# Optimization experiments

Measured on AMD Instinct MI355X. Metric: run time of the kernel, lower is better.

## Reference

```python
import jax, jax.numpy as jnp
import numpy as np

H = 128        # hidden_dim
NP = 512       # program nodes
NV = 50000     # voxel nodes
E = 800000     # cross edges (16 per voxel)
TAU = 1.0
SLOPE = 0.01   # LeakyReLU default negative slope


def setup_inputs() -> dict:
    key = jax.random.key(0)
    ks = jax.random.split(key, 12)
    s = 1.0 / np.sqrt(H)
    x = jax.random.normal(ks[0], (NP, H), dtype=jnp.float32)
    v = jax.random.normal(ks[1], (NV, H), dtype=jnp.float32)
    row0 = jax.random.randint(ks[2], (E,), 0, NP, dtype=jnp.int32)
    row1 = (jnp.arange(E, dtype=jnp.int32) % NV)  # every voxel gets E/NV edges
    cross_edge_index = jnp.stack([row0, row1])    # [2, E]
    W_program = jax.random.normal(ks[3], (H, H), dtype=jnp.float32) * s
    b_program = jnp.zeros((H,), dtype=jnp.float32)
    W_voxel = jax.random.normal(ks[4], (H, H), dtype=jnp.float32) * s
    b_voxel = jnp.zeros((H,), dtype=jnp.float32)
    W_m1 = jax.random.normal(ks[5], (H, H), dtype=jnp.float32) * s
    b_m1 = jnp.zeros((H,), dtype=jnp.float32)
    W_m2 = jax.random.normal(ks[6], (H, 1), dtype=jnp.float32) * s
    b_m2 = jnp.zeros((1,), dtype=jnp.float32)
    theta = jax.random.normal(ks[7], (H, 1), dtype=jnp.float32) * s  # xavier-like
    u = jax.random.uniform(ks[8], (E,), dtype=jnp.float32)
    gumbel_u = jnp.clip(u, 1e-7, 1.0 - 1e-7)  # avoid log(0)
    return {"x": x, "v": v, "cross_edge_index": cross_edge_index,
            "W_program": W_program, "b_program": b_program,
            "W_voxel": W_voxel, "b_voxel": b_voxel,
            "W_m1": W_m1, "b_m1": b_m1, "W_m2": W_m2, "b_m2": b_m2,
            "theta": theta, "gumbel_u": gumbel_u}


def reference(x, v, cross_edge_index, W_program, b_program, W_voxel, b_voxel,
              W_m1, b_m1, W_m2, b_m2, theta, gumbel_u):
    src = cross_edge_index[0]
    dst = cross_edge_index[1]
    x_sel = x[src]                      # [E, H] gather
    v_sel = v[dst]                      # [E, H] gather
    # mask = sigmoid(MLP(v)) : Linear -> LeakyReLU -> Linear(H,1)
    a = v @ W_m1 + b_m1
    a = jnp.where(a >= 0, a, SLOPE * a)
    mask = jax.nn.sigmoid(a @ W_m2 + b_m2)                  # [NV, 1]
    # attention logits: theta^T * tanh(Wp x_sel + Wv v_sel), summed over H
    t = jnp.tanh(x_sel @ W_program + b_program + v_sel @ W_voxel + b_voxel)
    e = jnp.sum(t * theta[:, 0], axis=-1)                   # [E]
    # Gumbel softmax: global softmax over all edges (dim=0 in torch on 1-D e)
    g = -jnp.log(-jnp.log(gumbel_u))
    y = jax.nn.softmax((e + g) / TAU)                       # [E]
    # per-voxel hard argmax (scatter_max), straight-through estimator
    seg_max = jax.ops.segment_max(y, dst, num_segments=NV)  # [NV]
    is_max = y == seg_max[dst]
    cand = jnp.where(is_max, jnp.arange(E), E)
    argmax = jax.ops.segment_min(cand, dst, num_segments=NV)  # [NV], first max per voxel
    y_hard_1 = jnp.zeros(E + 1, y.dtype).at[argmax].set(1.0)[:E]  # overflow slot for empty segments
    y_hard = jax.lax.stop_gradient(y_hard_1 - y) + y
    # scatter-sum of soft-attended program features back to voxels
    summed = jax.ops.segment_sum(x_sel * y[:, None], dst, num_segments=NV)  # [NV, H]
    v_out = v + mask * summed
    return (v_out, mask, y[:, None], y_hard[:, None])
```

## Files before the change

kernel.cpp:

```cpp
#include <hip/hip_runtime.h>

#define H     128
#define NP    512
#define NVOX  50000
#define NEDGE 800000
#define EPV   16
#define SLOPE 0.01f
#define GR    32
#define NBLK  ((NVOX + GR - 1) / GR)
#define STRH  136
#define VSTR  132
#define C1    2.8853900817779268f
#define LOG2E 1.4426950408889634f
#define LN2   0.6931471805599453f
#define ABLK  3125

#define EXP2(x) __builtin_amdgcn_exp2f(x)
#define LOG2(x) __builtin_amdgcn_logf(x)
#define RCP(x)  __builtin_amdgcn_rcpf(x)

typedef _Float16 h16;
typedef __attribute__((ext_vector_type(4))) _Float16 h16x4;
typedef __attribute__((ext_vector_type(8))) _Float16 h16x8;
typedef __attribute__((ext_vector_type(4))) float    f32x4;

__global__ __launch_bounds__(256) void k_pre(const float* __restrict__ x,
                                             const float* __restrict__ Wp,
                                             const float* __restrict__ bp,
                                             const float* __restrict__ Wv,
                                             const float* __restrict__ Wm1,
                                             float* __restrict__ xpout,
                                             h16* __restrict__ WvThi,
                                             h16* __restrict__ WvTlo,
                                             h16* __restrict__ Wm1T) {
    __shared__ float part[H];
    int bid = blockIdx.x;
    int tid = threadIdx.x;
    if (bid < NP) {
        int row = bid;
        int col = tid & 127;
        int kh  = tid >> 7;
        int kbase = kh * 64;
        const float* xr = x + (size_t)row * H;
        float acc = 0.f;
#pragma unroll 8
        for (int k = 0; k < 64; ++k)
            acc = fmaf(xr[kbase + k], Wp[(size_t)(kbase + k) * H + col], acc);
        if (kh == 1) part[col] = acc;
        __syncthreads();
        if (kh == 0) xpout[(size_t)row * H + col] = (acc + part[col] + bp[col]) * C1;
    } else {
        int idx = (bid - NP) * 256 + tid;
        if (idx < 16384) {
            int k = idx >> 7, n = idx & 127;
            float w = Wv[idx];
            h16 hi = (h16)w;
            WvThi[n * H + k] = hi;
            WvTlo[n * H + k] = (h16)(w - (float)hi);
        } else {
            int j = idx - 16384;
            int k = j >> 7, n = j & 127;
            Wm1T[n * H + k] = (h16)Wm1[j];
        }
    }
}

__global__ __launch_bounds__(256, 2) void k_main(
    const float* __restrict__ v,   const float* __restrict__ x,
    const float* __restrict__ bv,  const float* __restrict__ bm1,
    const float* __restrict__ Wm2, const float* __restrict__ bm2,
    const h16* __restrict__ WvThi, const h16* __restrict__ WvTlo,
    const h16* __restrict__ Wm1T,
    const float* __restrict__ xp,  const int* __restrict__ cei,
    const float* __restrict__ theta, const float* __restrict__ gum,
    float* __restrict__ mask_out, float* __restrict__ pout,
    float* __restrict__ sump,     float* __restrict__ partial)
{
    __shared__ __align__(16) char ldsbuf[GR * STRH * 2 * 2];
    h16*   vh = (h16*)ldsbuf;
    h16*   vl = vh + GR * STRH;
    float* vt = (float*)ldsbuf;
    __shared__ float pmbuf[4][GR];
    __shared__ float psums[4];
    __shared__ float ptile[EPV][GR];
    __shared__ int   amtile[GR];

    int tid  = threadIdx.x;
    int base = blockIdx.x * GR;

#pragma unroll
    for (int i = 0; i < 4; ++i) {
        int f  = i * 256 + tid;
        int r  = f >> 5, c4 = f & 31;
        int gr = base + r;
        float4 val = (gr < NVOX) ? *(const float4*)&v[(size_t)gr * H + c4 * 4]
                                 : make_float4(0.f, 0.f, 0.f, 0.f);
        h16x4 hi, lo;
        hi.x = (h16)val.x; lo.x = (h16)(val.x - (float)hi.x);
        hi.y = (h16)val.y; lo.y = (h16)(val.y - (float)hi.y);
        hi.z = (h16)val.z; lo.z = (h16)(val.z - (float)hi.z);
        hi.w = (h16)val.w; lo.w = (h16)(val.w - (float)hi.w);
        *(h16x4*)&vh[r * STRH + c4 * 4] = hi;
        *(h16x4*)&vl[r * STRH + c4 * 4] = lo;
    }
    __syncthreads();

    int wave = tid >> 6, lane = tid & 63;
    int m16 = lane & 15, quad = lane >> 4;
    int cb = wave * 32;

    f32x4 aV[2][2], aM[2][2];
#pragma unroll
    for (int rt = 0; rt < 2; ++rt)
#pragma unroll
        for (int ct = 0; ct < 2; ++ct) { aV[rt][ct] = (f32x4)0.f; aM[rt][ct] = (f32x4)0.f; }

#pragma unroll
    for (int kc = 0; kc < 4; ++kc) {
        int kofs = kc * 32 + quad * 8;
        h16x8 ah[2], al[2];
#pragma unroll
        for (int rt = 0; rt < 2; ++rt) {
            int row = rt * 16 + m16;
            ah[rt] = *(const h16x8*)&vh[row * STRH + kofs];
            al[rt] = *(const h16x8*)&vl[row * STRH + kofs];
        }
#pragma unroll
        for (int ct = 0; ct < 2; ++ct) {
            int n = cb + ct * 16 + m16;
            h16x8 bh = *(const h16x8*)&WvThi[n * H + kofs];
            h16x8 bl = *(const h16x8*)&WvTlo[n * H + kofs];
            h16x8 bm = *(const h16x8*)&Wm1T[n * H + kofs];
#pragma unroll
            for (int rt = 0; rt < 2; ++rt) {
                aV[rt][ct] = __builtin_amdgcn_mfma_f32_16x16x32_f16(ah[rt], bh, aV[rt][ct], 0, 0, 0);
                aV[rt][ct] = __builtin_amdgcn_mfma_f32_16x16x32_f16(al[rt], bh, aV[rt][ct], 0, 0, 0);
                aV[rt][ct] = __builtin_amdgcn_mfma_f32_16x16x32_f16(ah[rt], bl, aV[rt][ct], 0, 0, 0);
                aM[rt][ct] = __builtin_amdgcn_mfma_f32_16x16x32_f16(ah[rt], bm, aM[rt][ct], 0, 0, 0);
            }
        }
    }
    __syncthreads();

    float pml[2][4];
#pragma unroll
    for (int rt = 0; rt < 2; ++rt)
#pragma unroll
        for (int reg = 0; reg < 4; ++reg) pml[rt][reg] = 0.f;
#pragma unroll
    for (int ct = 0; ct < 2; ++ct) {
        int col = cb + ct * 16 + m16;
        float bvc = bv[col], bmc = bm1[col], w2c = Wm2[col];
#pragma unroll
        for (int rt = 0; rt < 2; ++rt)
#pragma unroll
            for (int reg = 0; reg < 4; ++reg) {
                int row = rt * 16 + quad * 4 + reg;
                vt[row * VSTR + col] = (aV[rt][ct][reg] + bvc) * C1;
                float m = aM[rt][ct][reg] + bmc;
                m = (m >= 0.f) ? m : SLOPE * m;
                pml[rt][reg] = fmaf(m, w2c, pml[rt][reg]);
            }
    }
#pragma unroll
    for (int off = 8; off >= 1; off >>= 1)
#pragma unroll
        for (int rt = 0; rt < 2; ++rt)
#pragma unroll
            for (int reg = 0; reg < 4; ++reg)
                pml[rt][reg] += __shfl_xor(pml[rt][reg], off, 64);
    if (m16 == 0) {
#pragma unroll
        for (int rt = 0; rt < 2; ++rt)
#pragma unroll
            for (int reg = 0; reg < 4; ++reg)
                pmbuf[wave][rt * 16 + quad * 4 + reg] = pml[rt][reg];
    }
    __syncthreads();
    if (wave == 0 && lane < GR) {
        int gr = base + lane;
        if (gr < NVOX) {
            float s = pmbuf[0][lane] + pmbuf[1][lane] + pmbuf[2][lane]
                    + pmbuf[3][lane] + bm2[0];
            mask_out[gr] = RCP(1.f + EXP2(-s * LOG2E));
        }
    }

    int g = tid >> 3, lk = tid & 7;
    float th2[16], thsum = 0.f;
#pragma unroll
    for (int i = 0; i < 4; ++i) {
        float4 t4 = *(const float4*)&theta[(lk + 8 * i) * 4];
        th2[i * 4 + 0] = -2.f * t4.x; th2[i * 4 + 1] = -2.f * t4.y;
        th2[i * 4 + 2] = -2.f * t4.z; th2[i * 4 + 3] = -2.f * t4.w;
        thsum += t4.x + t4.y + t4.z + t4.w;
    }
    int vox = base + g;
    bool valid = vox < NVOX;
    const float* vr = &vt[g * VSTR];
    float4 b0 = *(const float4*)&vr[(lk +  0) * 4];
    float4 b1 = *(const float4*)&vr[(lk +  8) * 4];
    float4 b2 = *(const float4*)&vr[(lk + 16) * 4];
    float4 b3 = *(const float4*)&vr[(lk + 24) * 4];

    float4 s0 = make_float4(0.f,0.f,0.f,0.f), s1 = s0, s2 = s0, s3 = s0;
    float psum = 0.f, pmax = -1.f;
    int   pidx = 0;
#pragma unroll 2
    for (int t = 0; t < EPV; ++t) {
        int e   = vox + t * NVOX;
        int src = valid ? cei[e] : 0;
        const float4* xr = (const float4*)(xp + (size_t)src * H);
        const float4* xo = (const float4*)(x  + (size_t)src * H);
        float4 a0 = xr[lk], a1 = xr[lk + 8], a2 = xr[lk + 16], a3 = xr[lk + 24];
        float4 c0 = xo[lk], c1 = xo[lk + 8], c2 = xo[lk + 16], c3 = xo[lk + 24];
        float acc0 = thsum, acc1 = 0.f;
        acc0 = fmaf(th2[ 0], RCP(EXP2(a0.x + b0.x) + 1.f), acc0);
        acc1 = fmaf(th2[ 1], RCP(EXP2(a0.y + b0.y) + 1.f), acc1);
        acc0 = fmaf(th2[ 2], RCP(EXP2(a0.z + b0.z) + 1.f), acc0);
        acc1 = fmaf(th2[ 3], RCP(EXP2(a0.w + b0.w) + 1.f), acc1);
        acc0 = fmaf(th2[ 4], RCP(EXP2(a1.x + b1.x) + 1.f), acc0);
        acc1 = fmaf(th2[ 5], RCP(EXP2(a1.y + b1.y) + 1.f), acc1);
        acc0 = fmaf(th2[ 6], RCP(EXP2(a1.z + b1.z) + 1.f), acc0);
        acc1 = fmaf(th2[ 7], RCP(EXP2(a1.w + b1.w) + 1.f), acc1);
        acc0 = fmaf(th2[ 8], RCP(EXP2(a2.x + b2.x) + 1.f), acc0);
        acc1 = fmaf(th2[ 9], RCP(EXP2(a2.y + b2.y) + 1.f), acc1);
        acc0 = fmaf(th2[10], RCP(EXP2(a2.z + b2.z) + 1.f), acc0);
        acc1 = fmaf(th2[11], RCP(EXP2(a2.w + b2.w) + 1.f), acc1);
        acc0 = fmaf(th2[12], RCP(EXP2(a3.x + b3.x) + 1.f), acc0);
        acc1 = fmaf(th2[13], RCP(EXP2(a3.y + b3.y) + 1.f), acc1);
        acc0 = fmaf(th2[14], RCP(EXP2(a3.z + b3.z) + 1.f), acc0);
        acc1 = fmaf(th2[15], RCP(EXP2(a3.w + b3.w) + 1.f), acc1);
        float acc = acc0 + acc1;
        acc += __shfl_xor(acc, 4, 64);
        acc += __shfl_xor(acc, 2, 64);
        acc += __shfl_xor(acc, 1, 64);
        float u  = gum[valid ? e : 0];
        float gm = -LN2 * LOG2(-LN2 * LOG2(u));
        float p  = EXP2((acc + gm) * LOG2E);
        if (p > pmax) { pmax = p; pidx = t; }
        psum += (lk == 0 && valid) ? p : 0.f;
        if (lk == 0) ptile[t][g] = p;
        s0.x = fmaf(p, c0.x, s0.x); s0.y = fmaf(p, c0.y, s0.y);
        s0.z = fmaf(p, c0.z, s0.z); s0.w = fmaf(p, c0.w, s0.w);
        s1.x = fmaf(p, c1.x, s1.x); s1.y = fmaf(p, c1.y, s1.y);
        s1.z = fmaf(p, c1.z, s1.z); s1.w = fmaf(p, c1.w, s1.w);
        s2.x = fmaf(p, c2.x, s2.x); s2.y = fmaf(p, c2.y, s2.y);
        s2.z = fmaf(p, c2.z, s2.z); s2.w = fmaf(p, c2.w, s2.w);
        s3.x = fmaf(p, c3.x, s3.x); s3.y = fmaf(p, c3.y, s3.y);
        s3.z = fmaf(p, c3.z, s3.z); s3.w = fmaf(p, c3.w, s3.w);
    }
    if (lk == 0) amtile[g] = pidx;
    if (valid) {
        float* sr = sump + (size_t)vox * H;
        *(float4*)&sr[(lk +  0) * 4] = s0;
        *(float4*)&sr[(lk +  8) * 4] = s1;
        *(float4*)&sr[(lk + 16) * 4] = s2;
        *(float4*)&sr[(lk + 24) * 4] = s3;
    }
    __syncthreads();
#pragma unroll
    for (int it = 0; it < 2; ++it) {
        int t = (tid >> 5) + 8 * it, c = tid & 31;
        int vox2 = base + c;
        if (vox2 < NVOX) {
            float val = ptile[t][c];
            pout[vox2 + t * NVOX] = (t == amtile[c]) ? -val : val;
        }
    }
#pragma unroll
    for (int off = 32; off >= 1; off >>= 1) psum += __shfl_xor(psum, off, 64);
    if (lane == 0) psums[wave] = psum;
    __syncthreads();
    if (tid == 0)
        partial[blockIdx.x] = psums[0] + psums[1] + psums[2] + psums[3];
}

__global__ __launch_bounds__(256) void k_out(const float* __restrict__ v,
                                             const float* __restrict__ maskp,
                                             const float* __restrict__ partial,
                                             float* __restrict__ vout,
                                             float* __restrict__ ybuf,
                                             float* __restrict__ yhard) {
    __shared__ float red[4];
    int tid = threadIdx.x;
    float s = 0.f;
    for (int i = tid; i < NBLK; i += 256) s += partial[i];
#pragma unroll
    for (int off = 32; off >= 1; off >>= 1) s += __shfl_xor(s, off, 64);
    if ((tid & 63) == 0) red[tid >> 6] = s;
    __syncthreads();
    float invS = RCP(red[0] + red[1] + red[2] + red[3]);

    int bid = blockIdx.x;
    if (bid < ABLK) {
#pragma unroll
        for (int r = 0; r < 2; ++r) {
            int i = (bid + r * ABLK) * 256 + tid;
            float4 sp = ((const float4*)vout)[i];
            float4 vv = ((const float4*)v)[i];
            float  m  = maskp[i >> 5] * invS;
            float4 o;
            o.x = fmaf(m, sp.x, vv.x); o.y = fmaf(m, sp.y, vv.y);
            o.z = fmaf(m, sp.z, vv.z); o.w = fmaf(m, sp.w, vv.w);
            ((float4*)vout)[i] = o;
        }
    } else {
        int e = (bid - ABLK) * 256 + tid;
        float pv = ybuf[e];
        ybuf[e]  = fabsf(pv) * invS;
        yhard[e] = (pv < 0.f) ? 1.f : 0.f;
    }
}

extern "C" void kernel_launch(void* const* d_in, const int* in_sizes, int n_in,
                              void* d_out, int out_size, void* d_ws, size_t ws_size,
                              hipStream_t stream) {
    (void)in_sizes; (void)n_in; (void)out_size; (void)ws_size;
    const float* x   = (const float*)d_in[0];
    const float* v   = (const float*)d_in[1];
    const int*   cei = (const int*)d_in[2];
    const float* Wp  = (const float*)d_in[3];
    const float* bp  = (const float*)d_in[4];
    const float* Wv  = (const float*)d_in[5];
    const float* bv  = (const float*)d_in[6];
    const float* Wm1 = (const float*)d_in[7];
    const float* bm1 = (const float*)d_in[8];
    const float* Wm2 = (const float*)d_in[9];
    const float* bm2 = (const float*)d_in[10];
    const float* th  = (const float*)d_in[11];
    const float* gum = (const float*)d_in[12];

    float* out   = (float*)d_out;
    float* vout  = out;
    float* maskp = out + (size_t)NVOX * H;
    float* ybuf  = maskp + NVOX;
    float* yhard = ybuf + NEDGE;
    float* xp    = yhard;
    h16*   WvThi = (h16*)(yhard + 65536);
    h16*   WvTlo = WvThi + 16384;
    h16*   Wm1T  = WvThi + 32768;
    float* partial = (float*)d_ws;

    k_pre<<<NP + 128, 256, 0, stream>>>(x, Wp, bp, Wv, Wm1, xp, WvThi, WvTlo, Wm1T);
    k_main<<<NBLK, 256, 0, stream>>>(v, x, bv, bm1, Wm2, bm2, WvThi, WvTlo, Wm1T,
                                     xp, cei, th, gum, maskp, ybuf, vout, partial);
    k_out<<<2 * ABLK, 256, 0, stream>>>(v, maskp, partial, vout, ybuf, yhard);
}
```

Measured before the change: 192.5 us.

## Halve voxels per block, split edges across thread halves, stage indices in LDS

Each block now handles 16 voxels instead of 32. The 16 edges per voxel are split between two halves of the block, and the two partial scatter sums are combined through shared memory. Edge indices and gumbel values are prefetched into LDS, and the gumbel term is folded into a multiplicative weight computed with fewer transcendentals. The partial-sum reduction moves out of every k_out block into a single k_reduce kernel. The aim is more blocks and more parallelism per voxel, at the cost of an extra launch, extra syncs, and dependence on NVOX being divisible by 16.

Result: slower. 197.4 us (+2.5%).

```diff
diff --git a/kernel.cpp b/kernel.cpp
--- a/kernel.cpp
+++ b/kernel.cpp
@@ -6,13 +6,12 @@
 #define NEDGE 800000
 #define EPV   16
 #define SLOPE 0.01f
-#define GR    32
-#define NBLK  ((NVOX + GR - 1) / GR)
+#define GR    16
+#define NBLK  (NVOX / GR)
 #define STRH  136
 #define VSTR  132
 #define C1    2.8853900817779268f
 #define LOG2E 1.4426950408889634f
-#define LN2   0.6931471805599453f
 #define ABLK  3125
 
 #define EXP2(x) __builtin_amdgcn_exp2f(x)
@@ -65,7 +64,7 @@
     }
 }
 
-__global__ __launch_bounds__(256, 2) void k_main(
+__global__ __launch_bounds__(256) void k_main(
     const float* __restrict__ v,   const float* __restrict__ x,
     const float* __restrict__ bv,  const float* __restrict__ bm1,
     const float* __restrict__ Wm2, const float* __restrict__ bm2,
@@ -76,25 +75,26 @@
     float* __restrict__ mask_out, float* __restrict__ pout,
     float* __restrict__ sump,     float* __restrict__ partial)
 {
-    __shared__ __align__(16) char ldsbuf[GR * STRH * 2 * 2];
-    h16*   vh = (h16*)ldsbuf;
-    h16*   vl = vh + GR * STRH;
-    float* vt = (float*)ldsbuf;
+    __shared__ __align__(16) char ldsbuf[2 * GR * STRH * 2];
+    h16*   vh   = (h16*)ldsbuf;
+    h16*   vl   = vh + GR * STRH;
+    float* vt   = (float*)ldsbuf;
+    float* scmb = (float*)ldsbuf;
+    __shared__ float ptile[EPV * GR];
+    __shared__ int   ceit[EPV * GR];
+    __shared__ float gumt[EPV * GR];
+    __shared__ int   amtile[GR];
     __shared__ float pmbuf[4][GR];
     __shared__ float psums[4];
-    __shared__ float ptile[EPV][GR];
-    __shared__ int   amtile[GR];
 
     int tid  = threadIdx.x;
     int base = blockIdx.x * GR;
 
 #pragma unroll
-    for (int i = 0; i < 4; ++i) {
+    for (int i = 0; i < 2; ++i) {
         int f  = i * 256 + tid;
         int r  = f >> 5, c4 = f & 31;
-        int gr = base + r;
-        float4 val = (gr < NVOX) ? *(const float4*)&v[(size_t)gr * H + c4 * 4]
-                                 : make_float4(0.f, 0.f, 0.f, 0.f);
+        float4 val = *(const float4*)&v[(size_t)(base + r) * H + c4 * 4];
         h16x4 hi, lo;
         hi.x = (h16)val.x; lo.x = (h16)(val.x - (float)hi.x);
         hi.y = (h16)val.y; lo.y = (h16)(val.y - (float)hi.y);
@@ -103,113 +103,98 @@
         *(h16x4*)&vh[r * STRH + c4 * 4] = hi;
         *(h16x4*)&vl[r * STRH + c4 * 4] = lo;
     }
+    {
+        int t = tid >> 4, c = tid & 15;
+        int e = base + c + t * NVOX;
+        ceit[tid] = cei[e];
+        gumt[tid] = gum[e];
+    }
     __syncthreads();
 
     int wave = tid >> 6, lane = tid & 63;
     int m16 = lane & 15, quad = lane >> 4;
     int cb = wave * 32;
 
-    f32x4 aV[2][2], aM[2][2];
-#pragma unroll
-    for (int rt = 0; rt < 2; ++rt)
-#pragma unroll
-        for (int ct = 0; ct < 2; ++ct) { aV[rt][ct] = (f32x4)0.f; aM[rt][ct] = (f32x4)0.f; }
+    f32x4 aV[2], aM[2];
+#pragma unroll
+    for (int ct = 0; ct < 2; ++ct) { aV[ct] = (f32x4)0.f; aM[ct] = (f32x4)0.f; }
 
 #pragma unroll
     for (int kc = 0; kc < 4; ++kc) {
         int kofs = kc * 32 + quad * 8;
-        h16x8 ah[2], al[2];
-#pragma unroll
-        for (int rt = 0; rt < 2; ++rt) {
-            int row = rt * 16 + m16;
-            ah[rt] = *(const h16x8*)&vh[row * STRH + kofs];
-            al[rt] = *(const h16x8*)&vl[row * STRH + kofs];
-        }
+        h16x8 ah = *(const h16x8*)&vh[m16 * STRH + kofs];
+        h16x8 al = *(const h16x8*)&vl[m16 * STRH + kofs];
 #pragma unroll
         for (int ct = 0; ct < 2; ++ct) {
             int n = cb + ct * 16 + m16;
             h16x8 bh = *(const h16x8*)&WvThi[n * H + kofs];
             h16x8 bl = *(const h16x8*)&WvTlo[n * H + kofs];
             h16x8 bm = *(const h16x8*)&Wm1T[n * H + kofs];
-#pragma unroll
-            for (int rt = 0; rt < 2; ++rt) {
-                aV[rt][ct] = __builtin_amdgcn_mfma_f32_16x16x32_f16(ah[rt], bh, aV[rt][ct], 0, 0, 0);
-                aV[rt][ct] = __builtin_amdgcn_mfma_f32_16x16x32_f16(al[rt], bh, aV[rt][ct], 0, 0, 0);
-                aV[rt][ct] = __builtin_amdgcn_mfma_f32_16x16x32_f16(ah[rt], bl, aV[rt][ct], 0, 0, 0);
-                aM[rt][ct] = __builtin_amdgcn_mfma_f32_16x16x32_f16(ah[rt], bm, aM[rt][ct], 0, 0, 0);
-            }
-        }
-    }
-    __syncthreads();
-
-    float pml[2][4];
-#pragma unroll
-    for (int rt = 0; rt < 2; ++rt)
-#pragma unroll
-        for (int reg = 0; reg < 4; ++reg) pml[rt][reg] = 0.f;
+            aV[ct] = __builtin_amdgcn_mfma_f32_16x16x32_f16(ah, bh, aV[ct], 0, 0, 0);
+            aV[ct] = __builtin_amdgcn_mfma_f32_16x16x32_f16(al, bh, aV[ct], 0, 0, 0);
+            aV[ct] = __builtin_amdgcn_mfma_f32_16x16x32_f16(ah, bl, aV[ct], 0, 0, 0);
+            aM[ct] = __builtin_amdgcn_mfma_f32_16x16x32_f16(ah, bm, aM[ct], 0, 0, 0);
+        }
+    }
+    __syncthreads();
+
+    float pml[4] = {0.f, 0.f, 0.f, 0.f};
 #pragma unroll
     for (int ct = 0; ct < 2; ++ct) {
         int col = cb + ct * 16 + m16;
         float bvc = bv[col], bmc = bm1[col], w2c = Wm2[col];
 #pragma unroll
-        for (int rt = 0; rt < 2; ++rt)
-#pragma unroll
-            for (int reg = 0; reg < 4; ++reg) {
-                int row = rt * 16 + quad * 4 + reg;
-                vt[row * VSTR + col] = (aV[rt][ct][reg] + bvc) * C1;
-                float m = aM[rt][ct][reg] + bmc;
-                m = (m >= 0.f) ? m : SLOPE * m;
-                pml[rt][reg] = fmaf(m, w2c, pml[rt][reg]);
-            }
+        for (int reg = 0; reg < 4; ++reg) {
+            int row = quad * 4 + reg;
+            vt[row * VSTR + col] = (aV[ct][reg] + bvc) * C1;
+            float m = aM[ct][reg] + bmc;
+            m = (m >= 0.f) ? m : SLOPE * m;
+            pml[reg] = fmaf(m, w2c, pml[reg]);
+        }
     }
 #pragma unroll
     for (int off = 8; off >= 1; off >>= 1)
 #pragma unroll
-        for (int rt = 0; rt < 2; ++rt)
-#pragma unroll
-            for (int reg = 0; reg < 4; ++reg)
-                pml[rt][reg] += __shfl_xor(pml[rt][reg], off, 64);
+        for (int reg = 0; reg < 4; ++reg)
+            pml[reg] += __shfl_xor(pml[reg], off, 64);
     if (m16 == 0) {
 #pragma unroll
-        for (int rt = 0; rt < 2; ++rt)
-#pragma unroll
-            for (int reg = 0; reg < 4; ++reg)
-                pmbuf[wave][rt * 16 + quad * 4 + reg] = pml[rt][reg];
+        for (int reg = 0; reg < 4; ++reg)
+            pmbuf[wave][quad * 4 + reg] = pml[reg];
     }
     __syncthreads();
     if (wave == 0 && lane < GR) {
-        int gr = base + lane;
-        if (gr < NVOX) {
-            float s = pmbuf[0][lane] + pmbuf[1][lane] + pmbuf[2][lane]
-                    + pmbuf[3][lane] + bm2[0];
-            mask_out[gr] = RCP(1.f + EXP2(-s * LOG2E));
-        }
+        float s = pmbuf[0][lane] + pmbuf[1][lane] + pmbuf[2][lane]
+                + pmbuf[3][lane] + bm2[0];
+        mask_out[base + lane] = RCP(1.f + EXP2(-s * LOG2E));
     }
 
     int g = tid >> 3, lk = tid & 7;
+    int vx = g & 15, half = g >> 4;
     float th2[16], thsum = 0.f;
 #pragma unroll
     for (int i = 0; i < 4; ++i) {
         float4 t4 = *(const float4*)&theta[(lk + 8 * i) * 4];
-        th2[i * 4 + 0] = -2.f * t4.x; th2[i * 4 + 1] = -2.f * t4.y;
-        th2[i * 4 + 2] = -2.f * t4.z; th2[i * 4 + 3] = -2.f * t4.w;
-        thsum += t4.x + t4.y + t4.z + t4.w;
-    }
-    int vox = base + g;
-    bool valid = vox < NVOX;
-    const float* vr = &vt[g * VSTR];
+        th2[i * 4 + 0] = -2.f * LOG2E * t4.x; th2[i * 4 + 1] = -2.f * LOG2E * t4.y;
+        th2[i * 4 + 2] = -2.f * LOG2E * t4.z; th2[i * 4 + 3] = -2.f * LOG2E * t4.w;
+        thsum += LOG2E * (t4.x + t4.y + t4.z + t4.w);
+    }
+    const float* vr = &vt[vx * VSTR];
     float4 b0 = *(const float4*)&vr[(lk +  0) * 4];
     float4 b1 = *(const float4*)&vr[(lk +  8) * 4];
     float4 b2 = *(const float4*)&vr[(lk + 16) * 4];
     float4 b3 = *(const float4*)&vr[(lk + 24) * 4];
+    float wv8[8];
+#pragma unroll
+    for (int i = 0; i < 8; ++i)
+        wv8[i] = -LOG2E * RCP(LOG2(gumt[(half * 8 + i) * GR + vx]));
+    __syncthreads();
 
     float4 s0 = make_float4(0.f,0.f,0.f,0.f), s1 = s0, s2 = s0, s3 = s0;
-    float psum = 0.f, pmax = -1.f;
-    int   pidx = 0;
 #pragma unroll 2
-    for (int t = 0; t < EPV; ++t) {
-        int e   = vox + t * NVOX;
-        int src = valid ? cei[e] : 0;
+    for (int i = 0; i < 8; ++i) {
+        int t   = half * 8 + i;
+        int src = ceit[t * GR + vx];
         const float4* xr = (const float4*)(xp + (size_t)src * H);
         const float4* xo = (const float4*)(x  + (size_t)src * H);
         float4 a0 = xr[lk], a1 = xr[lk + 8], a2 = xr[lk + 16], a3 = xr[lk + 24];
@@ -235,12 +220,8 @@
         acc += __shfl_xor(acc, 4, 64);
         acc += __shfl_xor(acc, 2, 64);
         acc += __shfl_xor(acc, 1, 64);
-        float u  = gum[valid ? e : 0];
-        float gm = -LN2 * LOG2(-LN2 * LOG2(u));
-        float p  = EXP2((acc + gm) * LOG2E);
-        if (p > pmax) { pmax = p; pidx = t; }
-        psum += (lk == 0 && valid) ? p : 0.f;
-        if (lk == 0) ptile[t][g] = p;
+        float p = EXP2(acc) * wv8[i];
+        if (lk == 0) ptile[t * GR + vx] = p;
         s0.x = fmaf(p, c0.x, s0.x); s0.y = fmaf(p, c0.y, s0.y);
         s0.z = fmaf(p, c0.z, s0.z); s0.w = fmaf(p, c0.w, s0.w);
         s1.x = fmaf(p, c1.x, s1.x); s1.y = fmaf(p, c1.y, s1.y);
@@ -250,24 +231,43 @@
         s3.x = fmaf(p, c3.x, s3.x); s3.y = fmaf(p, c3.y, s3.y);
         s3.z = fmaf(p, c3.z, s3.z); s3.w = fmaf(p, c3.w, s3.w);
     }
-    if (lk == 0) amtile[g] = pidx;
-    if (valid) {
-        float* sr = sump + (size_t)vox * H;
-        *(float4*)&sr[(lk +  0) * 4] = s0;
-        *(float4*)&sr[(lk +  8) * 4] = s1;
-        *(float4*)&sr[(lk + 16) * 4] = s2;
-        *(float4*)&sr[(lk + 24) * 4] = s3;
-    }
-    __syncthreads();
-#pragma unroll
-    for (int it = 0; it < 2; ++it) {
-        int t = (tid >> 5) + 8 * it, c = tid & 31;
-        int vox2 = base + c;
-        if (vox2 < NVOX) {
-            float val = ptile[t][c];
-            pout[vox2 + t * NVOX] = (t == amtile[c]) ? -val : val;
-        }
-    }
+    if (half == 1) {
+        float* sc = scmb + vx * 128;
+        *(float4*)&sc[(lk +  0) * 4] = s0;
+        *(float4*)&sc[(lk +  8) * 4] = s1;
+        *(float4*)&sc[(lk + 16) * 4] = s2;
+        *(float4*)&sc[(lk + 24) * 4] = s3;
+    }
+    __syncthreads();
+    if (tid < GR) {
+        float mx = ptile[tid]; int a = 0;
+#pragma unroll
+        for (int t = 1; t < EPV; ++t) {
+            float yv = ptile[t * GR + tid];
+            if (yv > mx) { mx = yv; a = t; }
+        }
+        amtile[tid] = a;
+    }
+    if (half == 0) {
+        const float* sc = scmb + vx * 128;
+        float4 r0 = *(const float4*)&sc[(lk +  0) * 4];
+        float4 r1 = *(const float4*)&sc[(lk +  8) * 4];
+        float4 r2 = *(const float4*)&sc[(lk + 16) * 4];
+        float4 r3 = *(const float4*)&sc[(lk + 24) * 4];
+        float* sr = sump + (size_t)(base + vx) * H;
+        *(float4*)&sr[(lk +  0) * 4] = make_float4(s0.x+r0.x, s0.y+r0.y, s0.z+r0.z, s0.w+r0.w);
+        *(float4*)&sr[(lk +  8) * 4] = make_float4(s1.x+r1.x, s1.y+r1.y, s1.z+r1.z, s1.w+r1.w);
+        *(float4*)&sr[(lk + 16) * 4] = make_float4(s2.x+r2.x, s2.y+r2.y, s2.z+r2.z, s2.w+r2.w);
+        *(float4*)&sr[(lk + 24) * 4] = make_float4(s3.x+r3.x, s3.y+r3.y, s3.z+r3.z, s3.w+r3.w);
+    }
+    __syncthreads();
+    float pv;
+    {
+        int t = tid >> 4, c = tid & 15;
+        pv = ptile[tid];
+        pout[base + c + t * NVOX] = (t == amtile[c]) ? -pv : pv;
+    }
+    float psum = pv;
 #pragma unroll
     for (int off = 32; off >= 1; off >>= 1) psum += __shfl_xor(psum, off, 64);
     if (lane == 0) psums[wave] = psum;
@@ -276,22 +276,27 @@
         partial[blockIdx.x] = psums[0] + psums[1] + psums[2] + psums[3];
 }
 
+__global__ __launch_bounds__(256) void k_reduce(const float* __restrict__ partial,
+                                                float* __restrict__ invS) {
+    __shared__ float wsum[4];
+    int tid = threadIdx.x;
+    float s = 0.f;
+    for (int i = tid; i < NBLK; i += 256) s += partial[i];
+#pragma unroll
+    for (int off = 32; off >= 1; off >>= 1) s += __shfl_xor(s, off, 64);
+    if ((tid & 63) == 0) wsum[tid >> 6] = s;
+    __syncthreads();
+    if (tid == 0) invS[0] = 1.f / (wsum[0] + wsum[1] + wsum[2] + wsum[3]);
+}
+
 __global__ __launch_bounds__(256) void k_out(const float* __restrict__ v,
                                              const float* __restrict__ maskp,
-                                             const float* __restrict__ partial,
+                                             const float* __restrict__ invSp,
                                              float* __restrict__ vout,
                                              float* __restrict__ ybuf,
                                              float* __restrict__ yhard) {
-    __shared__ float red[4];
+    float invS = invSp[0];
     int tid = threadIdx.x;
-    float s = 0.f;
-    for (int i = tid; i < NBLK; i += 256) s += partial[i];
-#pragma unroll
-    for (int off = 32; off >= 1; off >>= 1) s += __shfl_xor(s, off, 64);
-    if ((tid & 63) == 0) red[tid >> 6] = s;
-    __syncthreads();
-    float invS = RCP(red[0] + red[1] + red[2] + red[3]);
-
     int bid = blockIdx.x;
     if (bid < ABLK) {
 #pragma unroll
@@ -341,9 +346,11 @@
     h16*   WvTlo = WvThi + 16384;
     h16*   Wm1T  = WvThi + 32768;
     float* partial = (float*)d_ws;
+    float* invS    = (float*)d_ws + 4096;
 
     k_pre<<<NP + 128, 256, 0, stream>>>(x, Wp, bp, Wv, Wm1, xp, WvThi, WvTlo, Wm1T);
     k_main<<<NBLK, 256, 0, stream>>>(v, x, bv, bm1, Wm2, bm2, WvThi, WvTlo, Wm1T,
                                      xp, cei, th, gum, maskp, ybuf, vout, partial);
-    k_out<<<2 * ABLK, 256, 0, stream>>>(v, maskp, partial, vout, ybuf, yhard);
-}
+    k_reduce<<<1, 256, 0, stream>>>(partial, invS);
+    k_out<<<2 * ABLK, 256, 0, stream>>>(v, maskp, invS, vout, ybuf, yhard);
+}
```

## Prefetch next edge row, stage edge indices in LDS, simplify Gumbel math

Applied to the files above, without the earlier changes.

The edge loop now loads the next edge's projected program row while computing the current edge, so gather latency can overlap with the tanh and softmax math. Source indices and Gumbel noise for the block are loaded into shared memory up front, replacing per-iteration global loads. The Gumbel term uses exp(-log(-log u)) = -1/ln u, which drops one log and one exp per edge, and LOG2E is folded into theta. Launch bounds are raised to 4 blocks per CU; together with the extra prefetch registers this could cause spills or lower occupancy than intended.

Result: faster. 180.3 us (-6.4%).

```diff
diff --git a/kernel.cpp b/kernel.cpp
--- a/kernel.cpp
+++ b/kernel.cpp
@@ -7,12 +7,11 @@
 #define EPV   16
 #define SLOPE 0.01f
 #define GR    32
-#define NBLK  ((NVOX + GR - 1) / GR)
+#define NBLK  1563
 #define STRH  136
 #define VSTR  132
 #define C1    2.8853900817779268f
 #define LOG2E 1.4426950408889634f
-#define LN2   0.6931471805599453f
 #define ABLK  3125
 
 #define EXP2(x) __builtin_amdgcn_exp2f(x)
@@ -65,7 +64,7 @@
     }
 }
 
-__global__ __launch_bounds__(256, 2) void k_main(
+__global__ __launch_bounds__(256, 4) void k_mainX(
     const float* __restrict__ v,   const float* __restrict__ x,
     const float* __restrict__ bv,  const float* __restrict__ bm1,
     const float* __restrict__ Wm2, const float* __restrict__ bm2,
@@ -76,14 +75,16 @@
     float* __restrict__ mask_out, float* __restrict__ pout,
     float* __restrict__ sump,     float* __restrict__ partial)
 {
-    __shared__ __align__(16) char ldsbuf[GR * STRH * 2 * 2];
+    __shared__ __align__(16) char ldsbuf[2 * GR * STRH * 2];
     h16*   vh = (h16*)ldsbuf;
     h16*   vl = vh + GR * STRH;
     float* vt = (float*)ldsbuf;
+    __shared__ float ptile[EPV * GR];
+    __shared__ int   ceit[EPV * GR];
+    __shared__ float gumt[EPV * GR];
+    __shared__ int   amtile[GR];
     __shared__ float pmbuf[4][GR];
     __shared__ float psums[4];
-    __shared__ float ptile[EPV][GR];
-    __shared__ int   amtile[GR];
 
     int tid  = threadIdx.x;
     int base = blockIdx.x * GR;
@@ -92,9 +93,8 @@
     for (int i = 0; i < 4; ++i) {
         int f  = i * 256 + tid;
         int r  = f >> 5, c4 = f & 31;
-        int gr = base + r;
-        float4 val = (gr < NVOX) ? *(const float4*)&v[(size_t)gr * H + c4 * 4]
-                                 : make_float4(0.f, 0.f, 0.f, 0.f);
+        int gr = base + r; if (gr >= NVOX) gr = NVOX - 1;
+        float4 val = *(const float4*)&v[(size_t)gr * H + c4 * 4];
         h16x4 hi, lo;
         hi.x = (h16)val.x; lo.x = (h16)(val.x - (float)hi.x);
         hi.y = (h16)val.y; lo.y = (h16)(val.y - (float)hi.y);
@@ -103,6 +103,15 @@
         *(h16x4*)&vh[r * STRH + c4 * 4] = hi;
         *(h16x4*)&vl[r * STRH + c4 * 4] = lo;
     }
+#pragma unroll
+    for (int it = 0; it < 2; ++it) {
+        int idx = it * 256 + tid;
+        int t = idx >> 5, c = idx & 31;
+        int vx = base + c; if (vx >= NVOX) vx = NVOX - 1;
+        int e = vx + t * NVOX;
+        ceit[idx] = cei[e];
+        gumt[idx] = gum[e];
+    }
     __syncthreads();
 
     int wave = tid >> 6, lane = tid & 63;
@@ -187,16 +196,16 @@
     }
 
     int g = tid >> 3, lk = tid & 7;
+    int vox = base + g;
+    bool valid = vox < NVOX;
     float th2[16], thsum = 0.f;
 #pragma unroll
     for (int i = 0; i < 4; ++i) {
         float4 t4 = *(const float4*)&theta[(lk + 8 * i) * 4];
-        th2[i * 4 + 0] = -2.f * t4.x; th2[i * 4 + 1] = -2.f * t4.y;
-        th2[i * 4 + 2] = -2.f * t4.z; th2[i * 4 + 3] = -2.f * t4.w;
-        thsum += t4.x + t4.y + t4.z + t4.w;
-    }
-    int vox = base + g;
-    bool valid = vox < NVOX;
+        th2[i * 4 + 0] = -2.f * LOG2E * t4.x; th2[i * 4 + 1] = -2.f * LOG2E * t4.y;
+        th2[i * 4 + 2] = -2.f * LOG2E * t4.z; th2[i * 4 + 3] = -2.f * LOG2E * t4.w;
+        thsum += LOG2E * (t4.x + t4.y + t4.z + t4.w);
+    }
     const float* vr = &vt[g * VSTR];
     float4 b0 = *(const float4*)&vr[(lk +  0) * 4];
     float4 b1 = *(const float4*)&vr[(lk +  8) * 4];
@@ -206,14 +215,25 @@
     float4 s0 = make_float4(0.f,0.f,0.f,0.f), s1 = s0, s2 = s0, s3 = s0;
     float psum = 0.f, pmax = -1.f;
     int   pidx = 0;
-#pragma unroll 2
+
+    int srcC = ceit[g];
+    const float4* xr0 = (const float4*)(xp + (size_t)srcC * H);
+    float4 a0 = xr0[lk], a1 = xr0[lk + 8], a2 = xr0[lk + 16], a3 = xr0[lk + 24];
+
     for (int t = 0; t < EPV; ++t) {
-        int e   = vox + t * NVOX;
-        int src = valid ? cei[e] : 0;
-        const float4* xr = (const float4*)(xp + (size_t)src * H);
-        const float4* xo = (const float4*)(x  + (size_t)src * H);
-        float4 a0 = xr[lk], a1 = xr[lk + 8], a2 = xr[lk + 16], a3 = xr[lk + 24];
+        float4 n0, n1, n2, n3;
+        int srcN;
+        if (t < EPV - 1) {
+            srcN = ceit[(t + 1) * GR + g];
+            const float4* xrN = (const float4*)(xp + (size_t)srcN * H);
+            n0 = xrN[lk]; n1 = xrN[lk + 8]; n2 = xrN[lk + 16]; n3 = xrN[lk + 24];
+        } else {
+            srcN = srcC; n0 = a0; n1 = a1; n2 = a2; n3 = a3;
+        }
+        const float4* xo = (const float4*)(x + (size_t)srcC * H);
         float4 c0 = xo[lk], c1 = xo[lk + 8], c2 = xo[lk + 16], c3 = xo[lk + 24];
+        float wvt = -LOG2E * RCP(LOG2(gumt[t * GR + g]));
+
         float acc0 = thsum, acc1 = 0.f;
         acc0 = fmaf(th2[ 0], RCP(EXP2(a0.x + b0.x) + 1.f), acc0);
         acc1 = fmaf(th2[ 1], RCP(EXP2(a0.y + b0.y) + 1.f), acc1);
@@ -235,12 +255,10 @@
         acc += __shfl_xor(acc, 4, 64);
         acc += __shfl_xor(acc, 2, 64);
         acc += __shfl_xor(acc, 1, 64);
-        float u  = gum[valid ? e : 0];
-        float gm = -LN2 * LOG2(-LN2 * LOG2(u));
-        float p  = EXP2((acc + gm) * LOG2E);
+        float p = EXP2(acc) * wvt;
         if (p > pmax) { pmax = p; pidx = t; }
-        psum += (lk == 0 && valid) ? p : 0.f;
-        if (lk == 0) ptile[t][g] = p;
+        if (valid) psum += p;
+        if (lk == 0) ptile[t * GR + g] = p;
         s0.x = fmaf(p, c0.x, s0.x); s0.y = fmaf(p, c0.y, s0.y);
         s0.z = fmaf(p, c0.z, s0.z); s0.w = fmaf(p, c0.w, s0.w);
         s1.x = fmaf(p, c1.x, s1.x); s1.y = fmaf(p, c1.y, s1.y);
@@ -249,6 +267,7 @@
         s2.z = fmaf(p, c2.z, s2.z); s2.w = fmaf(p, c2.w, s2.w);
         s3.x = fmaf(p, c3.x, s3.x); s3.y = fmaf(p, c3.y, s3.y);
         s3.z = fmaf(p, c3.z, s3.z); s3.w = fmaf(p, c3.w, s3.w);
+        a0 = n0; a1 = n1; a2 = n2; a3 = n3; srcC = srcN;
     }
     if (lk == 0) amtile[g] = pidx;
     if (valid) {
@@ -258,20 +277,21 @@
         *(float4*)&sr[(lk + 16) * 4] = s2;
         *(float4*)&sr[(lk + 24) * 4] = s3;
     }
+    psum += __shfl_xor(psum, 8, 64);
+    psum += __shfl_xor(psum, 16, 64);
+    psum += __shfl_xor(psum, 32, 64);
+    if (lane == 0) psums[wave] = psum;
     __syncthreads();
 #pragma unroll
     for (int it = 0; it < 2; ++it) {
-        int t = (tid >> 5) + 8 * it, c = tid & 31;
+        int idx = it * 256 + tid;
+        int t = idx >> 5, c = idx & 31;
         int vox2 = base + c;
         if (vox2 < NVOX) {
-            float val = ptile[t][c];
+            float val = ptile[t * GR + c];
             pout[vox2 + t * NVOX] = (t == amtile[c]) ? -val : val;
         }
     }
-#pragma unroll
-    for (int off = 32; off >= 1; off >>= 1) psum += __shfl_xor(psum, off, 64);
-    if (lane == 0) psums[wave] = psum;
-    __syncthreads();
     if (tid == 0)
         partial[blockIdx.x] = psums[0] + psums[1] + psums[2] + psums[3];
 }
@@ -282,15 +302,15 @@
                                              float* __restrict__ vout,
                                              float* __restrict__ ybuf,
                                              float* __restrict__ yhard) {
-    __shared__ float red[4];
+    __shared__ float wsum[4];
     int tid = threadIdx.x;
     float s = 0.f;
     for (int i = tid; i < NBLK; i += 256) s += partial[i];
 #pragma unroll
     for (int off = 32; off >= 1; off >>= 1) s += __shfl_xor(s, off, 64);
-    if ((tid & 63) == 0) red[tid >> 6] = s;
-    __syncthreads();
-    float invS = RCP(red[0] + red[1] + red[2] + red[3]);
+    if ((tid & 63) == 0) wsum[tid >> 6] = s;
+    __syncthreads();
+    float invS = RCP(wsum[0] + wsum[1] + wsum[2] + wsum[3]);
 
     int bid = blockIdx.x;
     if (bid < ABLK) {
@@ -343,7 +363,7 @@
     float* partial = (float*)d_ws;
 
     k_pre<<<NP + 128, 256, 0, stream>>>(x, Wp, bp, Wv, Wm1, xp, WvThi, WvTlo, Wm1T);
-    k_main<<<NBLK, 256, 0, stream>>>(v, x, bv, bm1, Wm2, bm2, WvThi, WvTlo, Wm1T,
-                                     xp, cei, th, gum, maskp, ybuf, vout, partial);
+    k_mainX<<<NBLK, 256, 0, stream>>>(v, x, bv, bm1, Wm2, bm2, WvThi, WvTlo, Wm1T,
+                                      xp, cei, th, gum, maskp, ybuf, vout, partial);
     k_out<<<2 * ABLK, 256, 0, stream>>>(v, maskp, partial, vout, ybuf, yhard);
 }
```
